# Optimization experiments

Hardware: AMD Instinct MI355X
Metric: run time of the kernel (lower is better)

## Reference

```python
import jax, jax.numpy as jnp
import numpy as np

N = 100_000   # nodes
E = 1_000_000 # edges
F = 128       # nfeat
H = 2         # heads
C = 64        # nhid (per-head out channels)
NEG_SLOPE = 0.2
BN_EPS = 1e-5


def setup_inputs() -> dict:
    key = jax.random.key(0)
    ks = jax.random.split(key, 6)
    x = jax.random.normal(ks[0], (N, F), dtype=jnp.float32)
    edge_index = jax.random.randint(ks[1], (2, E), 0, N, dtype=jnp.int32)
    # GATConv params (xavier-ish scale)
    W = jax.random.normal(ks[2], (F, H * C), dtype=jnp.float32) * np.float32(1.0 / np.sqrt(F))
    att_src = jax.random.normal(ks[3], (H, C), dtype=jnp.float32) * np.float32(0.1)
    att_dst = jax.random.normal(ks[4], (H, C), dtype=jnp.float32) * np.float32(0.1)
    bias = jnp.zeros((H * C,), dtype=jnp.float32)
    # BatchNorm1d affine params
    gamma = jnp.ones((H * C,), dtype=jnp.float32)
    beta = jnp.zeros((H * C,), dtype=jnp.float32)
    return {"x": x, "edge_index": edge_index, "W": W, "att_src": att_src,
            "att_dst": att_dst, "bias": bias, "gamma": gamma, "beta": beta}


def reference(x, edge_index, W, att_src, att_dst, bias, gamma, beta):
    n = x.shape[0]
    # --- GATConv (PyG semantics): add self-loops, per-head linear, edge attention ---
    loop = jnp.arange(n, dtype=edge_index.dtype)
    src = jnp.concatenate([edge_index[0], loop])  # message sources (j)
    dst = jnp.concatenate([edge_index[1], loop])  # aggregation targets (i)

    h = (x @ W).reshape(n, H, C)                      # [N,H,C]
    a_src = jnp.einsum('nhc,hc->nh', h, att_src)      # [N,H]
    a_dst = jnp.einsum('nhc,hc->nh', h, att_dst)      # [N,H]

    e = jax.nn.leaky_relu(a_src[src] + a_dst[dst], NEG_SLOPE)  # [Et,H]
    # segment softmax over incoming edges of each dst node
    m = jax.lax.stop_gradient(jax.ops.segment_max(e, dst, num_segments=n))
    e = jnp.exp(e - m[dst])
    s = jax.ops.segment_sum(e, dst, num_segments=n)
    alpha = e / s[dst]                                 # [Et,H]

    out = jax.ops.segment_sum(alpha[:, :, None] * h[src], dst, num_segments=n)  # [N,H,C]
    out = out.reshape(n, H * C) + bias                 # concat heads + bias

    # --- transition: ReLU -> BatchNorm1d (training-mode batch stats) -> Dropout(eval=identity) ---
    out = jax.nn.relu(out)
    mean = out.mean(axis=0)
    var = out.var(axis=0)  # biased, as BN uses for normalization
    out = gamma * (out - mean) * jax.lax.rsqrt(var + BN_EPS) + beta
    return out
```

## Files before the change

kernel.cpp:

```cpp
#include <hip/hip_runtime.h>

#define NN 100000
#define EE 1000000
#define ET (EE + NN)
#define HC 128
#define NB 391
#define AGG_BLOCKS 2048
#define NGRP (NN / 4)
#define NTILE 6250

typedef __attribute__((ext_vector_type(8))) short short8;
typedef __attribute__((ext_vector_type(4))) float f32x4;

__device__ __forceinline__ unsigned bfpack(float a, float b) {
    unsigned ua = __float_as_uint(a), ub = __float_as_uint(b);
    ua += 0x7fff + ((ua >> 16) & 1);
    ub += 0x7fff + ((ub >> 16) & 1);
    return (ua >> 16) | (ub & 0xffff0000u);
}

__global__ __launch_bounds__(64) void k_wprep(const float* __restrict__ W,
                                              uint4* __restrict__ wf)
{
    const int bid = blockIdx.x;
    const int ks = bid >> 3, nt = bid & 7;
    const int l = threadIdx.x;
    const int n = nt * 16 + (l & 15);
    const int k0 = ks * 32 + (l >> 4) * 8;
    unsigned u[4];
    #pragma unroll
    for (int r = 0; r < 4; ++r)
        u[r] = bfpack(W[(k0 + 2*r) * HC + n], W[(k0 + 2*r + 1) * HC + n]);
    wf[bid * 64 + l] = make_uint4(u[0], u[1], u[2], u[3]);
}

__global__ __launch_bounds__(256) void k_gemm(
    const float* __restrict__ x, const uint4* __restrict__ wf,
    const float* __restrict__ atts, const float* __restrict__ attd,
    unsigned* __restrict__ hB, float2* __restrict__ asrc2, float2* __restrict__ adst2)
{
    __shared__ uint4 wl[2048];
    for (int i = threadIdx.x; i < 2048; i += 256) wl[i] = wf[i];
    __syncthreads();

    const int wv = threadIdx.x >> 6, lane = threadIdx.x & 63;
    const int g = lane >> 4, c15 = lane & 15;

    float As[8], Ad[8];
    #pragma unroll
    for (int nt = 0; nt < 8; ++nt) {
        As[nt] = atts[nt * 16 + c15];
        Ad[nt] = attd[nt * 16 + c15];
    }

    for (int t = blockIdx.x * 4 + wv; t < NTILE; t += gridDim.x * 4) {
        const int row0 = t * 16;
        union { unsigned u[4]; short8 v; } af[4];
        const float* xr = x + (size_t)(row0 + c15) * HC + g * 8;
        #pragma unroll
        for (int ks = 0; ks < 4; ++ks) {
            float4 lo = *(const float4*)(xr + ks * 32);
            float4 hi = *(const float4*)(xr + ks * 32 + 4);
            af[ks].u[0] = bfpack(lo.x, lo.y);
            af[ks].u[1] = bfpack(lo.z, lo.w);
            af[ks].u[2] = bfpack(hi.x, hi.y);
            af[ks].u[3] = bfpack(hi.z, hi.w);
        }
        f32x4 acc[8];
        #pragma unroll
        for (int nt = 0; nt < 8; ++nt) acc[nt] = (f32x4)(0.f);
        #pragma unroll
        for (int nt = 0; nt < 8; ++nt) {
            #pragma unroll
            for (int ks = 0; ks < 4; ++ks) {
                short8 bfr = *(const short8*)&wl[(ks * 8 + nt) * 64 + lane];
                acc[nt] = __builtin_amdgcn_mfma_f32_16x16x32_bf16(
                    af[ks].v, bfr, acc[nt], 0, 0, 0);
            }
        }
        #pragma unroll
        for (int r = 0; r < 4; ++r) {
            const int row = row0 + g * 4 + r;
            float ps = 0.f, pd = 0.f, qs = 0.f, qd = 0.f;
            #pragma unroll
            for (int nt = 0; nt < 4; ++nt) {
                float a = acc[nt][r], b = acc[nt + 4][r];
                hB[(size_t)row * 64 + nt * 16 + c15] = bfpack(a, b);
                ps += a * As[nt];     qs += a * Ad[nt];
                pd += b * As[nt + 4]; qd += b * Ad[nt + 4];
            }
            for (int off = 8; off; off >>= 1) {
                ps += __shfl_xor(ps, off); pd += __shfl_xor(pd, off);
                qs += __shfl_xor(qs, off); qd += __shfl_xor(qd, off);
            }
            if (c15 == 0) {
                asrc2[row] = make_float2(ps, pd);
                adst2[row] = make_float2(qs, qd);
            }
        }
    }
}

__device__ __forceinline__ void edge_sd(const int* __restrict__ ei, int t, int& s, int& d) {
    if (t < EE) { s = ei[t]; d = ei[EE + t]; }
    else        { s = t - EE; d = t - EE; }
}

__global__ __launch_bounds__(256) void k_hist(const int* __restrict__ ei,
                                              int* __restrict__ hist)
{
    int t = blockIdx.x * 256 + threadIdx.x;
    if (t >= ET) return;
    int d = (t < EE) ? ei[EE + t] : (t - EE);
    atomicAdd(&hist[d], 1);
}

__global__ __launch_bounds__(256) void k_scan1(const int* __restrict__ hist,
                                               int* __restrict__ part)
{
    __shared__ int ls[256];
    int i = blockIdx.x * 256 + threadIdx.x;
    ls[threadIdx.x] = (i < NN) ? hist[i] : 0;
    __syncthreads();
    for (int off = 128; off; off >>= 1) {
        if (threadIdx.x < off) ls[threadIdx.x] += ls[threadIdx.x + off];
        __syncthreads();
    }
    if (!threadIdx.x) part[blockIdx.x] = ls[0];
}

__global__ __launch_bounds__(512) void k_scan2(int* __restrict__ part)
{
    __shared__ int ls[512];
    int tid = threadIdx.x;
    int v = (tid < NB) ? part[tid] : 0;
    ls[tid] = v;
    __syncthreads();
    for (int off = 1; off < 512; off <<= 1) {
        int t = (tid >= off) ? ls[tid - off] : 0;
        __syncthreads();
        ls[tid] += t;
        __syncthreads();
    }
    if (tid < NB) part[tid] = ls[tid] - v;
}

__global__ __launch_bounds__(256) void k_scan3(const int* __restrict__ hist,
                                               const int* __restrict__ part,
                                               int* __restrict__ row_ptr)
{
    __shared__ int ls[256];
    int i = blockIdx.x * 256 + threadIdx.x;
    int v = (i < NN) ? hist[i] : 0;
    ls[threadIdx.x] = v;
    __syncthreads();
    for (int off = 1; off < 256; off <<= 1) {
        int t = (threadIdx.x >= off) ? ls[threadIdx.x - off] : 0;
        __syncthreads();
        ls[threadIdx.x] += t;
        __syncthreads();
    }
    if (i < NN) row_ptr[i] = part[blockIdx.x] + ls[threadIdx.x] - v;
    if (i == 0) row_ptr[NN] = ET;
}

__global__ __launch_bounds__(256) void k_bucket(
    const int* __restrict__ ei, const float* __restrict__ asrc,
    const float* __restrict__ adst, const int* __restrict__ row_ptr,
    int* __restrict__ cursor, int* __restrict__ csr_src, float2* __restrict__ pexp)
{
    int t = blockIdx.x * 256 + threadIdx.x;
    if (t >= ET) return;
    int s, d; edge_sd(ei, t, s, d);
    float2 av = *(const float2*)&asrc[s * 2];
    float2 dv = *(const float2*)&adst[d * 2];
    float e0 = av.x + dv.x; e0 = e0 > 0.f ? e0 : 0.2f * e0;
    float e1 = av.y + dv.y; e1 = e1 > 0.f ? e1 : 0.2f * e1;
    int pos = row_ptr[d] + atomicAdd(&cursor[d], 1);
    csr_src[pos] = s;
    pexp[pos] = make_float2(__expf(e0), __expf(e1));
}

__device__ __forceinline__ void gather8(const unsigned* base, const unsigned* off,
                                        unsigned* w) {
    asm volatile(
        "global_load_dword %0, %8,  %16\n\t"
        "global_load_dword %1, %9,  %16\n\t"
        "global_load_dword %2, %10, %16\n\t"
        "global_load_dword %3, %11, %16\n\t"
        "global_load_dword %4, %12, %16\n\t"
        "global_load_dword %5, %13, %16\n\t"
        "global_load_dword %6, %14, %16\n\t"
        "global_load_dword %7, %15, %16\n\t"
        "s_waitcnt vmcnt(0)"
        : "=&v"(w[0]), "=&v"(w[1]), "=&v"(w[2]), "=&v"(w[3]),
          "=&v"(w[4]), "=&v"(w[5]), "=&v"(w[6]), "=&v"(w[7])
        : "v"(off[0]), "v"(off[1]), "v"(off[2]), "v"(off[3]),
          "v"(off[4]), "v"(off[5]), "v"(off[6]), "v"(off[7]),
          "s"(base)
        : "memory");
}

__global__ __launch_bounds__(256) void k_agg(
    const int* __restrict__ row_ptr, const int* __restrict__ csr_src,
    const float2* __restrict__ pexp, const unsigned* __restrict__ hB,
    const float* __restrict__ bias,
    float* __restrict__ out, float* __restrict__ bpart)
{
    __shared__ float lsum[HC], lsq[HC];
    __shared__ int    lidx[4][64];
    __shared__ float2 lp[4][64];
    const int tid = threadIdx.x;
    if (tid < HC) { lsum[tid] = 0.f; lsq[tid] = 0.f; }
    __syncthreads();

    const int wv = tid >> 6, lane = tid & 63;
    const float b0c = bias[lane], b1c = bias[64 + lane];

    for (int g = blockIdx.x; g < NGRP; g += AGG_BLOCKS) {
        const int node = g * 4 + wv;
        const int beg = row_ptr[node], end = row_ptr[node + 1];

        float s0 = 0.f, s1 = 0.f;
        float acc0 = 0.f, acc1 = 0.f;

        for (int base = beg; base < end; base += 64) {
            const int cnt = min(64, end - base);
            if (lane < cnt) {
                float2 pv = pexp[base + lane];
                lidx[wv][lane] = csr_src[base + lane];
                lp[wv][lane] = pv;
                s0 += pv.x; s1 += pv.y;
            }
            for (int j0 = 0; j0 < cnt; j0 += 8) {
                unsigned off[8], w[8];
                float pwx[8], pwy[8];
                #pragma unroll
                for (int u = 0; u < 8; ++u) {
                    int j  = j0 + u;
                    int jc = j < cnt ? j : cnt - 1;
                    int s  = lidx[wv][jc];
                    float2 pv = lp[wv][jc];
                    pwx[u] = j < cnt ? pv.x : 0.f;
                    pwy[u] = j < cnt ? pv.y : 0.f;
                    off[u] = ((unsigned)s * 64u + (unsigned)lane) * 4u;
                }
                gather8(hB, off, w);
                #pragma unroll
                for (int u = 0; u < 8; ++u) {
                    acc0 = fmaf(pwx[u], __uint_as_float(w[u] << 16),         acc0);
                    acc1 = fmaf(pwy[u], __uint_as_float(w[u] & 0xffff0000u), acc1);
                }
            }
        }

        for (int off = 32; off; off >>= 1) {
            s0 += __shfl_xor(s0, off);
            s1 += __shfl_xor(s1, off);
        }

        float v0 = acc0 / s0 + b0c;  v0 = v0 > 0.f ? v0 : 0.f;
        float v1 = acc1 / s1 + b1c;  v1 = v1 > 0.f ? v1 : 0.f;
        out[(size_t)node * HC + lane]      = v0;
        out[(size_t)node * HC + 64 + lane] = v1;

        atomicAdd(&lsum[lane], v0);      atomicAdd(&lsq[lane], v0 * v0);
        atomicAdd(&lsum[64 + lane], v1); atomicAdd(&lsq[64 + lane], v1 * v1);
    }

    __syncthreads();
    bpart[(size_t)blockIdx.x * 256 + tid] = tid < HC ? lsum[tid] : lsq[tid - HC];
}

__global__ __launch_bounds__(256) void k_red(const float* __restrict__ bpart,
                                             float* __restrict__ p2)
{
    const int tid = threadIdx.x;
    float acc = 0.f;
    const int r0 = blockIdx.x * (AGG_BLOCKS / 16);
    #pragma unroll 4
    for (int r = 0; r < AGG_BLOCKS / 16; ++r)
        acc += bpart[(size_t)(r0 + r) * 256 + tid];
    p2[blockIdx.x * 256 + tid] = acc;
}

__global__ void k_bnparam(const float* __restrict__ p2,
                          const float* __restrict__ gamma, const float* __restrict__ beta,
                          float* __restrict__ scsh)
{
    int c = threadIdx.x;
    float sum = 0.f, sq = 0.f;
    #pragma unroll
    for (int i = 0; i < 16; ++i) {
        sum += p2[i * 256 + c];
        sq  += p2[i * 256 + c + 128];
    }
    float mean = sum * (1.f / NN);
    float var  = sq * (1.f / NN) - mean * mean;
    float sc   = gamma[c] * rsqrtf(var + 1e-5f);
    scsh[c]       = sc;
    scsh[128 + c] = beta[c] - mean * sc;
}

__global__ __launch_bounds__(256) void k_apply(float* __restrict__ out,
                                               const float* __restrict__ scsh)
{
    size_t i = (size_t)blockIdx.x * 256 + threadIdx.x;
    if (i * 4 >= (size_t)NN * HC) return;
    float4 v = ((float4*)out)[i];
    int c = (int)((i * 4) & (HC - 1));
    v.x = v.x * scsh[c]     + scsh[128 + c];
    v.y = v.y * scsh[c + 1] + scsh[128 + c + 1];
    v.z = v.z * scsh[c + 2] + scsh[128 + c + 2];
    v.w = v.w * scsh[c + 3] + scsh[128 + c + 3];
    ((float4*)out)[i] = v;
}

extern "C" void kernel_launch(void* const* d_in, const int* in_sizes, int n_in,
                              void* d_out, int out_size, void* d_ws, size_t ws_size,
                              hipStream_t stream) {
    const float* x     = (const float*)d_in[0];
    const int*   ei    = (const int*)  d_in[1];
    const float* W     = (const float*)d_in[2];
    const float* atts  = (const float*)d_in[3];
    const float* attd  = (const float*)d_in[4];
    const float* bias  = (const float*)d_in[5];
    const float* gamma = (const float*)d_in[6];
    const float* beta  = (const float*)d_in[7];
    float* out = (float*)d_out;
    float* ws  = (float*)d_ws;

    unsigned* hB     = (unsigned*)ws;
    float*    asrc   = ws + 6400000;
    float*    adst   = ws + 6600000;
    int*      hist   = (int*)(ws + 6800000);
    int*      cursor = (int*)(ws + 6900000);
    float*    scsh   = ws + 7000256;
    int*      row_ptr= (int*)(ws + 7000512);
    int*      part   = (int*)(ws + 7100513);
    int*      csr_src= (int*)(ws + 7101025);
    float2*   pexp   = (float2*)(ws + 8201026);
    float*    bpart  = ws + 10401026;
    float*    p2     = ws + 10925314;
    uint4*    wf     = (uint4*)(ws + 10929412);

    hipMemsetAsync(hist, 0, (size_t)200000 * sizeof(int), stream);

    k_wprep <<<32, 64, 0, stream>>>(W, wf);
    k_gemm  <<<782, 256, 0, stream>>>(x, wf, atts, attd, hB,
                                      (float2*)asrc, (float2*)adst);
    k_hist  <<<(ET + 255) / 256, 256, 0, stream>>>(ei, hist);
    k_scan1 <<<NB, 256, 0, stream>>>(hist, part);
    k_scan2 <<<1, 512, 0, stream>>>(part);
    k_scan3 <<<NB, 256, 0, stream>>>(hist, part, row_ptr);
    k_bucket<<<(ET + 255) / 256, 256, 0, stream>>>(ei, asrc, adst, row_ptr,
                                                   cursor, csr_src, pexp);
    k_agg   <<<AGG_BLOCKS, 256, 0, stream>>>(row_ptr, csr_src, pexp, hB, bias,
                                             out, bpart);
    k_red   <<<16, 256, 0, stream>>>(bpart, p2);
    k_bnparam<<<1, 128, 0, stream>>>(p2, gamma, beta, scsh);
    k_apply <<<(NN * HC / 4 + 255) / 256, 256, 0, stream>>>(out, scsh);
}
```

Before: 321.2 us.

## Compute edge attention in aggregation and gather two edges per wave with dwordx2 loads

The bucket kernel no longer reads asrc/adst or writes the per-edge exp weights. The aggregation kernel now recomputes them from asrc of each CSR source and adst of the node, which drops a 1.1M-entry float2 buffer write and read plus the random asrc/adst reads in the bucket pass. The gather loop is also restructured so each half-wave handles a different edge and each lane loads 8 bytes (two channel pairs). That halves the gather instruction count per edge, at the cost of a cross-half shuffle reduction and half the lanes idling in the epilogue.

```diff
diff --git a/kernel.cpp b/kernel.cpp
--- a/kernel.cpp
+++ b/kernel.cpp
@@ -165,33 +165,27 @@
 }
 
 __global__ __launch_bounds__(256) void k_bucket(
-    const int* __restrict__ ei, const float* __restrict__ asrc,
-    const float* __restrict__ adst, const int* __restrict__ row_ptr,
-    int* __restrict__ cursor, int* __restrict__ csr_src, float2* __restrict__ pexp)
+    const int* __restrict__ ei, const int* __restrict__ row_ptr,
+    int* __restrict__ cursor, int* __restrict__ csr_src)
 {
     int t = blockIdx.x * 256 + threadIdx.x;
     if (t >= ET) return;
     int s, d; edge_sd(ei, t, s, d);
-    float2 av = *(const float2*)&asrc[s * 2];
-    float2 dv = *(const float2*)&adst[d * 2];
-    float e0 = av.x + dv.x; e0 = e0 > 0.f ? e0 : 0.2f * e0;
-    float e1 = av.y + dv.y; e1 = e1 > 0.f ? e1 : 0.2f * e1;
     int pos = row_ptr[d] + atomicAdd(&cursor[d], 1);
     csr_src[pos] = s;
-    pexp[pos] = make_float2(__expf(e0), __expf(e1));
-}
-
-__device__ __forceinline__ void gather8(const unsigned* base, const unsigned* off,
-                                        unsigned* w) {
+}
+
+__device__ __forceinline__ void gather8x2(const unsigned* base, const unsigned* off,
+                                          unsigned long long* w) {
     asm volatile(
-        "global_load_dword %0, %8,  %16\n\t"
-        "global_load_dword %1, %9,  %16\n\t"
-        "global_load_dword %2, %10, %16\n\t"
-        "global_load_dword %3, %11, %16\n\t"
-        "global_load_dword %4, %12, %16\n\t"
-        "global_load_dword %5, %13, %16\n\t"
-        "global_load_dword %6, %14, %16\n\t"
-        "global_load_dword %7, %15, %16\n\t"
+        "global_load_dwordx2 %0, %8,  %16\n\t"
+        "global_load_dwordx2 %1, %9,  %16\n\t"
+        "global_load_dwordx2 %2, %10, %16\n\t"
+        "global_load_dwordx2 %3, %11, %16\n\t"
+        "global_load_dwordx2 %4, %12, %16\n\t"
+        "global_load_dwordx2 %5, %13, %16\n\t"
+        "global_load_dwordx2 %6, %14, %16\n\t"
+        "global_load_dwordx2 %7, %15, %16\n\t"
         "s_waitcnt vmcnt(0)"
         : "=&v"(w[0]), "=&v"(w[1]), "=&v"(w[2]), "=&v"(w[3]),
           "=&v"(w[4]), "=&v"(w[5]), "=&v"(w[6]), "=&v"(w[7])
@@ -203,8 +197,8 @@
 
 __global__ __launch_bounds__(256) void k_agg(
     const int* __restrict__ row_ptr, const int* __restrict__ csr_src,
-    const float2* __restrict__ pexp, const unsigned* __restrict__ hB,
-    const float* __restrict__ bias,
+    const float2* __restrict__ asrc2, const float2* __restrict__ adst2,
+    const unsigned* __restrict__ hB, const float* __restrict__ bias,
     float* __restrict__ out, float* __restrict__ bpart)
 {
     __shared__ float lsum[HC], lsq[HC];
@@ -215,57 +209,76 @@
     __syncthreads();
 
     const int wv = tid >> 6, lane = tid & 63;
-    const float b0c = bias[lane], b1c = bias[64 + lane];
+    const int half = lane >> 5, m = lane & 31;
+    const float bA0 = bias[2*m],      bB0 = bias[2*m + 1];
+    const float bA1 = bias[2*m + 64], bB1 = bias[2*m + 65];
 
     for (int g = blockIdx.x; g < NGRP; g += AGG_BLOCKS) {
         const int node = g * 4 + wv;
         const int beg = row_ptr[node], end = row_ptr[node + 1];
+        const float2 ad = adst2[node];
 
         float s0 = 0.f, s1 = 0.f;
-        float acc0 = 0.f, acc1 = 0.f;
+        float a0 = 0.f, a1 = 0.f, b0 = 0.f, b1 = 0.f;
 
         for (int base = beg; base < end; base += 64) {
             const int cnt = min(64, end - base);
             if (lane < cnt) {
-                float2 pv = pexp[base + lane];
-                lidx[wv][lane] = csr_src[base + lane];
+                int s = csr_src[base + lane];
+                float2 av = asrc2[s];
+                float e0 = av.x + ad.x; e0 = e0 > 0.f ? e0 : 0.2f * e0;
+                float e1 = av.y + ad.y; e1 = e1 > 0.f ? e1 : 0.2f * e1;
+                float2 pv = make_float2(__expf(e0), __expf(e1));
+                lidx[wv][lane] = s;
                 lp[wv][lane] = pv;
                 s0 += pv.x; s1 += pv.y;
             }
-            for (int j0 = 0; j0 < cnt; j0 += 8) {
-                unsigned off[8], w[8];
-                float pwx[8], pwy[8];
+            for (int j0 = 0; j0 < cnt; j0 += 16) {
+                unsigned off[8]; unsigned long long w[8];
+                float px[8], py[8];
                 #pragma unroll
                 for (int u = 0; u < 8; ++u) {
-                    int j  = j0 + u;
+                    int j  = j0 + 2 * u + half;
                     int jc = j < cnt ? j : cnt - 1;
                     int s  = lidx[wv][jc];
                     float2 pv = lp[wv][jc];
-                    pwx[u] = j < cnt ? pv.x : 0.f;
-                    pwy[u] = j < cnt ? pv.y : 0.f;
-                    off[u] = ((unsigned)s * 64u + (unsigned)lane) * 4u;
+                    px[u] = j < cnt ? pv.x : 0.f;
+                    py[u] = j < cnt ? pv.y : 0.f;
+                    off[u] = ((unsigned)s * 64u + (unsigned)m * 2u) * 4u;
                 }
-                gather8(hB, off, w);
+                gather8x2(hB, off, w);
                 #pragma unroll
                 for (int u = 0; u < 8; ++u) {
-                    acc0 = fmaf(pwx[u], __uint_as_float(w[u] << 16),         acc0);
-                    acc1 = fmaf(pwy[u], __uint_as_float(w[u] & 0xffff0000u), acc1);
+                    unsigned wlo = (unsigned)w[u];
+                    unsigned whi = (unsigned)(w[u] >> 32);
+                    a0 = fmaf(px[u], __uint_as_float(wlo << 16),          a0);
+                    a1 = fmaf(py[u], __uint_as_float(wlo & 0xffff0000u),  a1);
+                    b0 = fmaf(px[u], __uint_as_float(whi << 16),          b0);
+                    b1 = fmaf(py[u], __uint_as_float(whi & 0xffff0000u),  b1);
                 }
             }
         }
 
-        for (int off = 32; off; off >>= 1) {
-            s0 += __shfl_xor(s0, off);
-            s1 += __shfl_xor(s1, off);
-        }
-
-        float v0 = acc0 / s0 + b0c;  v0 = v0 > 0.f ? v0 : 0.f;
-        float v1 = acc1 / s1 + b1c;  v1 = v1 > 0.f ? v1 : 0.f;
-        out[(size_t)node * HC + lane]      = v0;
-        out[(size_t)node * HC + 64 + lane] = v1;
-
-        atomicAdd(&lsum[lane], v0);      atomicAdd(&lsq[lane], v0 * v0);
-        atomicAdd(&lsum[64 + lane], v1); atomicAdd(&lsq[64 + lane], v1 * v1);
+        a0 += __shfl_xor(a0, 32); a1 += __shfl_xor(a1, 32);
+        b0 += __shfl_xor(b0, 32); b1 += __shfl_xor(b1, 32);
+        for (int o = 32; o; o >>= 1) {
+            s0 += __shfl_xor(s0, o);
+            s1 += __shfl_xor(s1, o);
+        }
+        const float i0 = 1.f / s0, i1 = 1.f / s1;
+
+        if (half == 0) {
+            float vA0 = a0 * i0 + bA0; vA0 = vA0 > 0.f ? vA0 : 0.f;
+            float vB0 = b0 * i0 + bB0; vB0 = vB0 > 0.f ? vB0 : 0.f;
+            float vA1 = a1 * i1 + bA1; vA1 = vA1 > 0.f ? vA1 : 0.f;
+            float vB1 = b1 * i1 + bB1; vB1 = vB1 > 0.f ? vB1 : 0.f;
+            *(float2*)&out[(size_t)node * HC + 2*m]      = make_float2(vA0, vB0);
+            *(float2*)&out[(size_t)node * HC + 64 + 2*m] = make_float2(vA1, vB1);
+            atomicAdd(&lsum[2*m],      vA0); atomicAdd(&lsq[2*m],      vA0 * vA0);
+            atomicAdd(&lsum[2*m + 1],  vB0); atomicAdd(&lsq[2*m + 1],  vB0 * vB0);
+            atomicAdd(&lsum[2*m + 64], vA1); atomicAdd(&lsq[2*m + 64], vA1 * vA1);
+            atomicAdd(&lsum[2*m + 65], vB1); atomicAdd(&lsq[2*m + 65], vB1 * vB1);
+        }
     }
 
     __syncthreads();
@@ -339,7 +352,6 @@
     int*      row_ptr= (int*)(ws + 7000512);
     int*      part   = (int*)(ws + 7100513);
     int*      csr_src= (int*)(ws + 7101025);
-    float2*   pexp   = (float2*)(ws + 8201026);
     float*    bpart  = ws + 10401026;
     float*    p2     = ws + 10925314;
     uint4*    wf     = (uint4*)(ws + 10929412);
@@ -353,10 +365,10 @@
     k_scan1 <<<NB, 256, 0, stream>>>(hist, part);
     k_scan2 <<<1, 512, 0, stream>>>(part);
     k_scan3 <<<NB, 256, 0, stream>>>(hist, part, row_ptr);
-    k_bucket<<<(ET + 255) / 256, 256, 0, stream>>>(ei, asrc, adst, row_ptr,
-                                                   cursor, csr_src, pexp);
-    k_agg   <<<AGG_BLOCKS, 256, 0, stream>>>(row_ptr, csr_src, pexp, hB, bias,
-                                             out, bpart);
+    k_bucket<<<(ET + 255) / 256, 256, 0, stream>>>(ei, row_ptr, cursor, csr_src);
+    k_agg   <<<AGG_BLOCKS, 256, 0, stream>>>(row_ptr, csr_src,
+                                             (const float2*)asrc, (const float2*)adst,
+                                             hB, bias, out, bpart);
     k_red   <<<16, 256, 0, stream>>>(bpart, p2);
     k_bnparam<<<1, 128, 0, stream>>>(p2, gamma, beta, scsh);
     k_apply <<<(NN * HC / 4 + 255) / 256, 256, 0, stream>>>(out, scsh);
```

Measured after the change: 340.1 us. 5.9% more time.
